# Kernel tuning notes

Measured on AMD Instinct MI355X. Metric: run time of the kernel, lower is better.

## Reference

```python
import jax, jax.numpy as jnp
import numpy as np

N_NODES = 8192
F_DIM = 64
A_DIM = 8
HID = 32
AVG_DEG = 16.0


def _linear_params(key, fan_in, fan_out):
    # torch nn.Linear default init: U(-1/sqrt(fan_in), 1/sqrt(fan_in))
    s = 1.0 / np.sqrt(fan_in)
    k1, k2 = jax.random.split(key)
    W = jax.random.uniform(k1, (fan_in, fan_out), minval=-s, maxval=s, dtype=jnp.float32)
    b = jax.random.uniform(k2, (fan_out,), minval=-s, maxval=s, dtype=jnp.float32)
    return W, b


def setup_inputs() -> dict:
    key = jax.random.key(0)
    ks = jax.random.split(key, 12)
    N, Fd, Ad, H = N_NODES, F_DIM, A_DIM, HID

    features = jax.random.normal(ks[0], (N, Fd), dtype=jnp.float32)
    # sparse symmetric binary adjacency, zero diagonal (edge weights are discarded
    # by the original code -> all edges weight 1, so binary is the faithful form)
    u = jax.random.uniform(ks[1], (N, N), dtype=jnp.float32)
    adj = (u < AVG_DEG / N).astype(jnp.float32)
    adj = jnp.maximum(adj, adj.T) * (1.0 - jnp.eye(N, dtype=jnp.float32))
    mask = jax.random.uniform(ks[2], (N,), dtype=jnp.float32)  # RL_indice (unused)
    action = jax.random.normal(ks[3], (N, Ad), dtype=jnp.float32)

    We1, be1 = _linear_params(ks[4], Fd + Ad, H)
    We2, be2 = _linear_params(ks[5], H, H)
    Wg, bg = _linear_params(ks[6], H, H)      # GCNConv weight + bias
    Wgd, bgd = _linear_params(ks[7], H, H)    # GraphConv_Dense
    Wp1, bp1 = _linear_params(ks[8], 2 * H, H)
    Wp2, bp2 = _linear_params(ks[9], H, H)
    Wv, bv = _linear_params(ks[10], H, 1)

    return dict(features=features, adjacency=adjacency_fix(adj), mask=mask, action=action,
                We1=We1, be1=be1, We2=We2, be2=be2, Wg=Wg, bg=bg, Wgd=Wgd, bgd=bgd,
                Wp1=Wp1, bp1=bp1, Wp2=Wp2, bp2=bp2, Wv=Wv, bv=bv)


def adjacency_fix(adj):
    return adj


def reference(features, adjacency, mask, action,
              We1, be1, We2, be2, Wg, bg, Wgd, bgd,
              Wp1, bp1, Wp2, bp2, Wv, bv):
    # encoder
    X = jax.nn.relu(jnp.concatenate([features, action], axis=1) @ We1 + be1)  # [N,32]
    X = jax.nn.relu(X @ We2 + be2)                                            # [N,32]

    # GCNConv: out = D^{-1/2} (A + I) D^{-1/2} (X W) + b   (self-loops added, deg incl. self)
    deg = jnp.sum(adjacency, axis=1) + 1.0                 # [N]
    dinv = jax.lax.rsqrt(deg)                              # [N]
    S = (X @ Wg) * dinv[:, None]                           # [N,32] scaled messages
    Xg = (adjacency @ S + S) * dinv[:, None] + bg          # aggregate (A@S) + self-loop (S)
    Xg = jax.nn.relu(Xg)
    Xg = jax.nn.relu(Xg @ Wgd + bgd)

    # policy/value head on [graph || encoder] features
    P = jnp.concatenate([Xg, X], axis=1)                   # [N,64]
    P = jax.nn.relu(P @ Wp1 + bp1)
    P = jax.nn.relu(P @ Wp2 + bp2)
    V = P @ Wv + bv                                        # [N,1]
    return V
```

## Files before the change

### kernel.cpp

```cpp
#include <hip/hip_runtime.h>
#include <math.h>

#define NN 8192
#define FD 64
#define AD 8
#define H  32
#define CAP 128

typedef unsigned short u16;

__global__ __launch_bounds__(256) void scan_k(const float4* __restrict__ adj,
                                              u16* __restrict__ nbr,
                                              int* __restrict__ cnt,
                                              float* __restrict__ dinv) {
    const int row = blockIdx.x;
    const float4* arow = adj + (size_t)row * (NN / 4);
    __shared__ int s_cnt;
    if (threadIdx.x == 0) s_cnt = 0;
    __syncthreads();
    u16* myn = nbr + (size_t)row * CAP;

#pragma unroll
    for (int it = 0; it < NN / 4 / 256; ++it) {
        const int i4 = it * 256 + threadIdx.x;
        const float4 v = arow[i4];
        const int nz0 = (v.x != 0.0f), nz1 = (v.y != 0.0f);
        const int nz2 = (v.z != 0.0f), nz3 = (v.w != 0.0f);
        const int local = nz0 + nz1 + nz2 + nz3;
        if (local) {
            int slot = atomicAdd(&s_cnt, local);
            const int base = i4 * 4;
            if (slot + local <= CAP) {
                if (nz0) myn[slot++] = (u16)(base);
                if (nz1) myn[slot++] = (u16)(base + 1);
                if (nz2) myn[slot++] = (u16)(base + 2);
                if (nz3) myn[slot++] = (u16)(base + 3);
            }
        }
    }
    __syncthreads();
    if (threadIdx.x == 0) {
        int c = s_cnt;
        cnt[row]  = (c < CAP) ? c : CAP;
        dinv[row] = 1.0f / sqrtf((float)c + 1.0f);
    }
}

__global__ __launch_bounds__(256) void enc_k(const float* __restrict__ feat,
                                             const float* __restrict__ act,
                                             const float* __restrict__ We1,
                                             const float* __restrict__ be1,
                                             const float* __restrict__ We2,
                                             const float* __restrict__ be2,
                                             const float* __restrict__ Wg,
                                             const float* __restrict__ dinv,
                                             float* __restrict__ X,
                                             float* __restrict__ S) {
    __shared__ float sW1[(FD + AD) * H];
    __shared__ float sb1[H];
    __shared__ float sW2[H * H];
    __shared__ float sb2[H];
    __shared__ float sWg[H * H];
    for (int i = threadIdx.x; i < (FD + AD) * H; i += 256) sW1[i] = We1[i];
    for (int i = threadIdx.x; i < H * H; i += 256) { sW2[i] = We2[i]; sWg[i] = Wg[i]; }
    if (threadIdx.x < H) { sb1[threadIdx.x] = be1[threadIdx.x]; sb2[threadIdx.x] = be2[threadIdx.x]; }
    __syncthreads();

    const int row = blockIdx.x * 256 + threadIdx.x;

    float in[FD + AD];
    const float4* f4 = (const float4*)(feat + (size_t)row * FD);
#pragma unroll
    for (int i = 0; i < FD / 4; ++i) {
        float4 v = f4[i];
        in[4 * i] = v.x; in[4 * i + 1] = v.y; in[4 * i + 2] = v.z; in[4 * i + 3] = v.w;
    }
    const float4* a4 = (const float4*)(act + (size_t)row * AD);
#pragma unroll
    for (int i = 0; i < AD / 4; ++i) {
        float4 v = a4[i];
        in[FD + 4 * i] = v.x; in[FD + 4 * i + 1] = v.y;
        in[FD + 4 * i + 2] = v.z; in[FD + 4 * i + 3] = v.w;
    }

    float h1[H];
#pragma unroll
    for (int o = 0; o < H; ++o) h1[o] = sb1[o];
#pragma unroll
    for (int i = 0; i < FD + AD; ++i) {
        const float xi = in[i];
#pragma unroll
        for (int o = 0; o < H; ++o) h1[o] = fmaf(xi, sW1[i * H + o], h1[o]);
    }
#pragma unroll
    for (int o = 0; o < H; ++o) h1[o] = fmaxf(h1[o], 0.0f);

    float h2[H];
#pragma unroll
    for (int o = 0; o < H; ++o) h2[o] = sb2[o];
#pragma unroll
    for (int i = 0; i < H; ++i) {
        const float xi = h1[i];
#pragma unroll
        for (int o = 0; o < H; ++o) h2[o] = fmaf(xi, sW2[i * H + o], h2[o]);
    }
#pragma unroll
    for (int o = 0; o < H; ++o) h2[o] = fmaxf(h2[o], 0.0f);

    float* Xr = X + (size_t)row * H;
#pragma unroll
    for (int o = 0; o < H; o += 4)
        *(float4*)(Xr + o) = make_float4(h2[o], h2[o + 1], h2[o + 2], h2[o + 3]);

    float t[H];
#pragma unroll
    for (int o = 0; o < H; ++o) t[o] = 0.0f;
#pragma unroll
    for (int i = 0; i < H; ++i) {
        const float xi = h2[i];
#pragma unroll
        for (int o = 0; o < H; ++o) t[o] = fmaf(xi, sWg[i * H + o], t[o]);
    }
    const float di = dinv[row];
    float* Sr = S + (size_t)row * H;
#pragma unroll
    for (int o = 0; o < H; o += 4)
        *(float4*)(Sr + o) = make_float4(t[o] * di, t[o + 1] * di, t[o + 2] * di, t[o + 3] * di);
}

__global__ __launch_bounds__(256) void fin_k(const float* __restrict__ S,
                                             const float* __restrict__ X,
                                             const u16* __restrict__ nbr,
                                             const int* __restrict__ cnt,
                                             const float* __restrict__ dinv,
                                             const float* __restrict__ bg,
                                             const float* __restrict__ Wgd,
                                             const float* __restrict__ bgd,
                                             const float* __restrict__ Wp1,
                                             const float* __restrict__ bp1,
                                             const float* __restrict__ Wp2,
                                             const float* __restrict__ bp2,
                                             const float* __restrict__ Wv,
                                             const float* __restrict__ bv,
                                             float* __restrict__ out) {
    __shared__ float sbg[H];
    __shared__ float sWgd[H * H];
    __shared__ float sbgd[H];
    __shared__ float sWp1[2 * H * H];
    __shared__ float sbp1[H];
    __shared__ float sWp2[H * H];
    __shared__ float sbp2[H];
    __shared__ float sWv[H];
    __shared__ float sbv;
    for (int i = threadIdx.x; i < H * H; i += 256) { sWgd[i] = Wgd[i]; sWp2[i] = Wp2[i]; }
    for (int i = threadIdx.x; i < 2 * H * H; i += 256) sWp1[i] = Wp1[i];
    if (threadIdx.x < H) {
        sbg[threadIdx.x]  = bg[threadIdx.x];
        sbgd[threadIdx.x] = bgd[threadIdx.x];
        sbp1[threadIdx.x] = bp1[threadIdx.x];
        sbp2[threadIdx.x] = bp2[threadIdx.x];
        sWv[threadIdx.x]  = Wv[threadIdx.x];
    }
    if (threadIdx.x == 0) sbv = bv[0];
    __syncthreads();

    const int row = blockIdx.x * 256 + threadIdx.x;

    float acc[H];
    const float4* Sr = (const float4*)(S + (size_t)row * H);
#pragma unroll
    for (int q = 0; q < H / 4; ++q) {
        float4 v = Sr[q];
        acc[4 * q] = v.x; acc[4 * q + 1] = v.y; acc[4 * q + 2] = v.z; acc[4 * q + 3] = v.w;
    }
    const int n = cnt[row];
    const u16* myn = nbr + (size_t)row * CAP;
    for (int e = 0; e < n; ++e) {
        const int j = myn[e];
        const float4* Sj = (const float4*)(S + (size_t)j * H);
#pragma unroll
        for (int q = 0; q < H / 4; ++q) {
            float4 v = Sj[q];
            acc[4 * q] += v.x; acc[4 * q + 1] += v.y;
            acc[4 * q + 2] += v.z; acc[4 * q + 3] += v.w;
        }
    }

    const float di = dinv[row];
    float xg[H];
#pragma unroll
    for (int k = 0; k < H; ++k) xg[k] = fmaxf(fmaf(acc[k], di, sbg[k]), 0.0f);

    float xg2[H];
#pragma unroll
    for (int o = 0; o < H; ++o) xg2[o] = sbgd[o];
#pragma unroll
    for (int k = 0; k < H; ++k) {
        const float xk = xg[k];
#pragma unroll
        for (int o = 0; o < H; ++o) xg2[o] = fmaf(xk, sWgd[k * H + o], xg2[o]);
    }
#pragma unroll
    for (int o = 0; o < H; ++o) xg2[o] = fmaxf(xg2[o], 0.0f);

    float x[H];
    const float4* Xr = (const float4*)(X + (size_t)row * H);
#pragma unroll
    for (int q = 0; q < H / 4; ++q) {
        float4 v = Xr[q];
        x[4 * q] = v.x; x[4 * q + 1] = v.y; x[4 * q + 2] = v.z; x[4 * q + 3] = v.w;
    }

    float p1[H];
#pragma unroll
    for (int o = 0; o < H; ++o) p1[o] = sbp1[o];
#pragma unroll
    for (int k = 0; k < H; ++k) {
        const float xk = xg2[k];
#pragma unroll
        for (int o = 0; o < H; ++o) p1[o] = fmaf(xk, sWp1[k * H + o], p1[o]);
    }
#pragma unroll
    for (int k = 0; k < H; ++k) {
        const float xk = x[k];
#pragma unroll
        for (int o = 0; o < H; ++o) p1[o] = fmaf(xk, sWp1[(H + k) * H + o], p1[o]);
    }
#pragma unroll
    for (int o = 0; o < H; ++o) p1[o] = fmaxf(p1[o], 0.0f);

    float p2[H];
#pragma unroll
    for (int o = 0; o < H; ++o) p2[o] = sbp2[o];
#pragma unroll
    for (int k = 0; k < H; ++k) {
        const float xk = p1[k];
#pragma unroll
        for (int o = 0; o < H; ++o) p2[o] = fmaf(xk, sWp2[k * H + o], p2[o]);
    }

    float v = sbv;
#pragma unroll
    for (int k = 0; k < H; ++k) v = fmaf(fmaxf(p2[k], 0.0f), sWv[k], v);

    out[row] = v;
}

extern "C" void kernel_launch(void* const* d_in, const int* in_sizes, int n_in,
                              void* d_out, int out_size, void* d_ws, size_t ws_size,
                              hipStream_t stream) {
    (void)in_sizes; (void)n_in; (void)out_size; (void)ws_size;

    const float* feat = (const float*)d_in[0];
    const float* adj  = (const float*)d_in[1];
    const float* act  = (const float*)d_in[3];
    const float* We1  = (const float*)d_in[4];
    const float* be1  = (const float*)d_in[5];
    const float* We2  = (const float*)d_in[6];
    const float* be2  = (const float*)d_in[7];
    const float* Wg   = (const float*)d_in[8];
    const float* bg   = (const float*)d_in[9];
    const float* Wgd  = (const float*)d_in[10];
    const float* bgd  = (const float*)d_in[11];
    const float* Wp1  = (const float*)d_in[12];
    const float* bp1  = (const float*)d_in[13];
    const float* Wp2  = (const float*)d_in[14];
    const float* bp2  = (const float*)d_in[15];
    const float* Wv   = (const float*)d_in[16];
    const float* bv   = (const float*)d_in[17];

    char* ws = (char*)d_ws;
    u16*   nbr  = (u16*)ws;
    char*  p    = ws + (size_t)NN * CAP * sizeof(u16);
    int*   cnt  = (int*)p;            p += (size_t)NN * 4;
    float* dinv = (float*)p;          p += (size_t)NN * 4;
    float* X    = (float*)p;          p += (size_t)NN * H * 4;
    float* S    = (float*)p;

    float* out = (float*)d_out;

    scan_k<<<NN, 256, 0, stream>>>((const float4*)adj, nbr, cnt, dinv);
    enc_k<<<NN / 256, 256, 0, stream>>>(feat, act, We1, be1, We2, be2, Wg, dinv, X, S);
    fin_k<<<NN / 256, 256, 0, stream>>>(S, X, nbr, cnt, dinv, bg, Wgd, bgd,
                                        Wp1, bp1, Wp2, bp2, Wv, bv, out);
}
```

Baseline: 528.2 us.

## Merge adjacency scan and encoder into one launch, apply dinv during aggregation

Folds the adjacency scan and the encoder MLP into a single kernel: the first NN blocks scan adjacency rows and the extra blocks run the encoder. This works because the encoder no longer needs dinv, since the scaling by dinv[j] moves into the neighbor gather in fin_k. The scan also preloads all eight float4 loads per thread before processing them, to raise memory-level parallelism. fin_k drops to 64-thread blocks so more blocks spread across CUs, at the cost of an extra dinv load per edge.

```diff
diff --git a/kernel.cpp b/kernel.cpp
--- a/kernel.cpp
+++ b/kernel.cpp
@@ -9,140 +9,151 @@
 
 typedef unsigned short u16;
 
-__global__ __launch_bounds__(256) void scan_k(const float4* __restrict__ adj,
-                                              u16* __restrict__ nbr,
-                                              int* __restrict__ cnt,
-                                              float* __restrict__ dinv) {
-    const int row = blockIdx.x;
-    const float4* arow = adj + (size_t)row * (NN / 4);
-    __shared__ int s_cnt;
-    if (threadIdx.x == 0) s_cnt = 0;
-    __syncthreads();
-    u16* myn = nbr + (size_t)row * CAP;
-
-#pragma unroll
-    for (int it = 0; it < NN / 4 / 256; ++it) {
-        const int i4 = it * 256 + threadIdx.x;
-        const float4 v = arow[i4];
-        const int nz0 = (v.x != 0.0f), nz1 = (v.y != 0.0f);
-        const int nz2 = (v.z != 0.0f), nz3 = (v.w != 0.0f);
-        const int local = nz0 + nz1 + nz2 + nz3;
-        if (local) {
-            int slot = atomicAdd(&s_cnt, local);
-            const int base = i4 * 4;
-            if (slot + local <= CAP) {
-                if (nz0) myn[slot++] = (u16)(base);
-                if (nz1) myn[slot++] = (u16)(base + 1);
-                if (nz2) myn[slot++] = (u16)(base + 2);
-                if (nz3) myn[slot++] = (u16)(base + 3);
-            }
-        }
-    }
-    __syncthreads();
-    if (threadIdx.x == 0) {
-        int c = s_cnt;
-        cnt[row]  = (c < CAP) ? c : CAP;
-        dinv[row] = 1.0f / sqrtf((float)c + 1.0f);
-    }
-}
-
-__global__ __launch_bounds__(256) void enc_k(const float* __restrict__ feat,
+#define OW1 0
+#define OW2 2304
+#define OWG 3328
+#define OB1 4352
+#define OB2 4384
+#define SMEM_FLOATS 4416
+
+__global__ __launch_bounds__(256) void pre_k(const float4* __restrict__ adj,
+                                             const float* __restrict__ feat,
                                              const float* __restrict__ act,
                                              const float* __restrict__ We1,
                                              const float* __restrict__ be1,
                                              const float* __restrict__ We2,
                                              const float* __restrict__ be2,
                                              const float* __restrict__ Wg,
-                                             const float* __restrict__ dinv,
+                                             u16* __restrict__ nbr,
+                                             int* __restrict__ cnt,
+                                             float* __restrict__ dinv,
                                              float* __restrict__ X,
-                                             float* __restrict__ S) {
-    __shared__ float sW1[(FD + AD) * H];
-    __shared__ float sb1[H];
-    __shared__ float sW2[H * H];
-    __shared__ float sb2[H];
-    __shared__ float sWg[H * H];
-    for (int i = threadIdx.x; i < (FD + AD) * H; i += 256) sW1[i] = We1[i];
-    for (int i = threadIdx.x; i < H * H; i += 256) { sW2[i] = We2[i]; sWg[i] = Wg[i]; }
-    if (threadIdx.x < H) { sb1[threadIdx.x] = be1[threadIdx.x]; sb2[threadIdx.x] = be2[threadIdx.x]; }
-    __syncthreads();
-
-    const int row = blockIdx.x * 256 + threadIdx.x;
-
-    float in[FD + AD];
-    const float4* f4 = (const float4*)(feat + (size_t)row * FD);
-#pragma unroll
-    for (int i = 0; i < FD / 4; ++i) {
-        float4 v = f4[i];
-        in[4 * i] = v.x; in[4 * i + 1] = v.y; in[4 * i + 2] = v.z; in[4 * i + 3] = v.w;
-    }
-    const float4* a4 = (const float4*)(act + (size_t)row * AD);
-#pragma unroll
-    for (int i = 0; i < AD / 4; ++i) {
-        float4 v = a4[i];
-        in[FD + 4 * i] = v.x; in[FD + 4 * i + 1] = v.y;
-        in[FD + 4 * i + 2] = v.z; in[FD + 4 * i + 3] = v.w;
-    }
-
-    float h1[H];
-#pragma unroll
-    for (int o = 0; o < H; ++o) h1[o] = sb1[o];
-#pragma unroll
-    for (int i = 0; i < FD + AD; ++i) {
-        const float xi = in[i];
-#pragma unroll
-        for (int o = 0; o < H; ++o) h1[o] = fmaf(xi, sW1[i * H + o], h1[o]);
-    }
-#pragma unroll
-    for (int o = 0; o < H; ++o) h1[o] = fmaxf(h1[o], 0.0f);
-
-    float h2[H];
-#pragma unroll
-    for (int o = 0; o < H; ++o) h2[o] = sb2[o];
-#pragma unroll
-    for (int i = 0; i < H; ++i) {
-        const float xi = h1[i];
-#pragma unroll
-        for (int o = 0; o < H; ++o) h2[o] = fmaf(xi, sW2[i * H + o], h2[o]);
-    }
-#pragma unroll
-    for (int o = 0; o < H; ++o) h2[o] = fmaxf(h2[o], 0.0f);
-
-    float* Xr = X + (size_t)row * H;
-#pragma unroll
-    for (int o = 0; o < H; o += 4)
-        *(float4*)(Xr + o) = make_float4(h2[o], h2[o + 1], h2[o + 2], h2[o + 3]);
-
-    float t[H];
-#pragma unroll
-    for (int o = 0; o < H; ++o) t[o] = 0.0f;
-#pragma unroll
-    for (int i = 0; i < H; ++i) {
-        const float xi = h2[i];
-#pragma unroll
-        for (int o = 0; o < H; ++o) t[o] = fmaf(xi, sWg[i * H + o], t[o]);
-    }
-    const float di = dinv[row];
-    float* Sr = S + (size_t)row * H;
-#pragma unroll
-    for (int o = 0; o < H; o += 4)
-        *(float4*)(Sr + o) = make_float4(t[o] * di, t[o + 1] * di, t[o + 2] * di, t[o + 3] * di);
+                                             float* __restrict__ T) {
+    __shared__ float smem[SMEM_FLOATS];
+
+    if (blockIdx.x < NN) {
+        int* s_cnt = (int*)smem;
+        const int row = blockIdx.x;
+        const float4* arow = adj + (size_t)row * (NN / 4);
+        if (threadIdx.x == 0) *s_cnt = 0;
+        __syncthreads();
+
+        float4 v[8];
+#pragma unroll
+        for (int it = 0; it < 8; ++it) v[it] = arow[it * 256 + threadIdx.x];
+
+        u16* myn = nbr + (size_t)row * CAP;
+#pragma unroll
+        for (int it = 0; it < 8; ++it) {
+            const int base = (it * 256 + threadIdx.x) * 4;
+            const int nz0 = (v[it].x != 0.0f), nz1 = (v[it].y != 0.0f);
+            const int nz2 = (v[it].z != 0.0f), nz3 = (v[it].w != 0.0f);
+            const int local = nz0 + nz1 + nz2 + nz3;
+            if (local) {
+                int slot = atomicAdd(s_cnt, local);
+                if (slot + local <= CAP) {
+                    if (nz0) myn[slot++] = (u16)(base);
+                    if (nz1) myn[slot++] = (u16)(base + 1);
+                    if (nz2) myn[slot++] = (u16)(base + 2);
+                    if (nz3) myn[slot++] = (u16)(base + 3);
+                }
+            }
+        }
+        __syncthreads();
+        if (threadIdx.x == 0) {
+            const int c = *s_cnt;
+            cnt[row]  = (c < CAP) ? c : CAP;
+            dinv[row] = 1.0f / sqrtf((float)c + 1.0f);
+        }
+    } else {
+        for (int i = threadIdx.x; i < (FD + AD) * H; i += 256) smem[OW1 + i] = We1[i];
+        for (int i = threadIdx.x; i < H * H; i += 256) {
+            smem[OW2 + i] = We2[i];
+            smem[OWG + i] = Wg[i];
+        }
+        if (threadIdx.x < H) {
+            smem[OB1 + threadIdx.x] = be1[threadIdx.x];
+            smem[OB2 + threadIdx.x] = be2[threadIdx.x];
+        }
+        __syncthreads();
+
+        const int row = (blockIdx.x - NN) * 256 + threadIdx.x;
+
+        float in[FD + AD];
+        const float4* f4 = (const float4*)(feat + (size_t)row * FD);
+#pragma unroll
+        for (int i = 0; i < FD / 4; ++i) {
+            float4 v = f4[i];
+            in[4 * i] = v.x; in[4 * i + 1] = v.y; in[4 * i + 2] = v.z; in[4 * i + 3] = v.w;
+        }
+        const float4* a4 = (const float4*)(act + (size_t)row * AD);
+#pragma unroll
+        for (int i = 0; i < AD / 4; ++i) {
+            float4 v = a4[i];
+            in[FD + 4 * i] = v.x; in[FD + 4 * i + 1] = v.y;
+            in[FD + 4 * i + 2] = v.z; in[FD + 4 * i + 3] = v.w;
+        }
+
+        float h1[H];
+#pragma unroll
+        for (int o = 0; o < H; ++o) h1[o] = smem[OB1 + o];
+#pragma unroll
+        for (int i = 0; i < FD + AD; ++i) {
+            const float xi = in[i];
+#pragma unroll
+            for (int o = 0; o < H; ++o) h1[o] = fmaf(xi, smem[OW1 + i * H + o], h1[o]);
+        }
+#pragma unroll
+        for (int o = 0; o < H; ++o) h1[o] = fmaxf(h1[o], 0.0f);
+
+        float h2[H];
+#pragma unroll
+        for (int o = 0; o < H; ++o) h2[o] = smem[OB2 + o];
+#pragma unroll
+        for (int i = 0; i < H; ++i) {
+            const float xi = h1[i];
+#pragma unroll
+            for (int o = 0; o < H; ++o) h2[o] = fmaf(xi, smem[OW2 + i * H + o], h2[o]);
+        }
+#pragma unroll
+        for (int o = 0; o < H; ++o) h2[o] = fmaxf(h2[o], 0.0f);
+
+        float* Xr = X + (size_t)row * H;
+#pragma unroll
+        for (int o = 0; o < H; o += 4)
+            *(float4*)(Xr + o) = make_float4(h2[o], h2[o + 1], h2[o + 2], h2[o + 3]);
+
+        float t[H];
+#pragma unroll
+        for (int o = 0; o < H; ++o) t[o] = 0.0f;
+#pragma unroll
+        for (int i = 0; i < H; ++i) {
+            const float xi = h2[i];
+#pragma unroll
+            for (int o = 0; o < H; ++o) t[o] = fmaf(xi, smem[OWG + i * H + o], t[o]);
+        }
+        float* Tr = T + (size_t)row * H;
+#pragma unroll
+        for (int o = 0; o < H; o += 4)
+            *(float4*)(Tr + o) = make_float4(t[o], t[o + 1], t[o + 2], t[o + 3]);
+    }
 }
 
-__global__ __launch_bounds__(256) void fin_k(const float* __restrict__ S,
-                                             const float* __restrict__ X,
-                                             const u16* __restrict__ nbr,
-                                             const int* __restrict__ cnt,
-                                             const float* __restrict__ dinv,
-                                             const float* __restrict__ bg,
-                                             const float* __restrict__ Wgd,
-                                             const float* __restrict__ bgd,
-                                             const float* __restrict__ Wp1,
-                                             const float* __restrict__ bp1,
-                                             const float* __restrict__ Wp2,
-                                             const float* __restrict__ bp2,
-                                             const float* __restrict__ Wv,
-                                             const float* __restrict__ bv,
-                                             float* __restrict__ out) {
+__global__ __launch_bounds__(64) void fin_k(const float* __restrict__ T,
+                                            const float* __restrict__ X,
+                                            const u16* __restrict__ nbr,
+                                            const int* __restrict__ cnt,
+                                            const float* __restrict__ dinv,
+                                            const float* __restrict__ bg,
+                                            const float* __restrict__ Wgd,
+                                            const float* __restrict__ bgd,
+                                            const float* __restrict__ Wp1,
+                                            const float* __restrict__ bp1,
+                                            const float* __restrict__ Wp2,
+                                            const float* __restrict__ bp2,
+                                            const float* __restrict__ Wv,
+                                            const float* __restrict__ bv,
+                                            float* __restrict__ out) {
     __shared__ float sbg[H];
     __shared__ float sWgd[H * H];
     __shared__ float sbgd[H];
@@ -152,8 +163,8 @@
     __shared__ float sbp2[H];
     __shared__ float sWv[H];
     __shared__ float sbv;
-    for (int i = threadIdx.x; i < H * H; i += 256) { sWgd[i] = Wgd[i]; sWp2[i] = Wp2[i]; }
-    for (int i = threadIdx.x; i < 2 * H * H; i += 256) sWp1[i] = Wp1[i];
+    for (int i = threadIdx.x; i < H * H; i += 64) { sWgd[i] = Wgd[i]; sWp2[i] = Wp2[i]; }
+    for (int i = threadIdx.x; i < 2 * H * H; i += 64) sWp1[i] = Wp1[i];
     if (threadIdx.x < H) {
         sbg[threadIdx.x]  = bg[threadIdx.x];
         sbgd[threadIdx.x] = bgd[threadIdx.x];
@@ -164,29 +175,33 @@
     if (threadIdx.x == 0) sbv = bv[0];
     __syncthreads();
 
-    const int row = blockIdx.x * 256 + threadIdx.x;
+    const int row = blockIdx.x * 64 + threadIdx.x;
+    const float di = dinv[row];
 
     float acc[H];
-    const float4* Sr = (const float4*)(S + (size_t)row * H);
+    const float4* Tr = (const float4*)(T + (size_t)row * H);
 #pragma unroll
     for (int q = 0; q < H / 4; ++q) {
-        float4 v = Sr[q];
-        acc[4 * q] = v.x; acc[4 * q + 1] = v.y; acc[4 * q + 2] = v.z; acc[4 * q + 3] = v.w;
+        float4 v = Tr[q];
+        acc[4 * q]     = v.x * di; acc[4 * q + 1] = v.y * di;
+        acc[4 * q + 2] = v.z * di; acc[4 * q + 3] = v.w * di;
     }
     const int n = cnt[row];
     const u16* myn = nbr + (size_t)row * CAP;
     for (int e = 0; e < n; ++e) {
         const int j = myn[e];
-        const float4* Sj = (const float4*)(S + (size_t)j * H);
+        const float dj = dinv[j];
+        const float4* Tj = (const float4*)(T + (size_t)j * H);
 #pragma unroll
         for (int q = 0; q < H / 4; ++q) {
-            float4 v = Sj[q];
-            acc[4 * q] += v.x; acc[4 * q + 1] += v.y;
-            acc[4 * q + 2] += v.z; acc[4 * q + 3] += v.w;
-        }
-    }
-
-    const float di = dinv[row];
+            float4 v = Tj[q];
+            acc[4 * q]     = fmaf(v.x, dj, acc[4 * q]);
+            acc[4 * q + 1] = fmaf(v.y, dj, acc[4 * q + 1]);
+            acc[4 * q + 2] = fmaf(v.z, dj, acc[4 * q + 2]);
+            acc[4 * q + 3] = fmaf(v.w, dj, acc[4 * q + 3]);
+        }
+    }
+
     float xg[H];
 #pragma unroll
     for (int k = 0; k < H; ++k) xg[k] = fmaxf(fmaf(acc[k], di, sbg[k]), 0.0f);
@@ -275,12 +290,13 @@
     int*   cnt  = (int*)p;            p += (size_t)NN * 4;
     float* dinv = (float*)p;          p += (size_t)NN * 4;
     float* X    = (float*)p;          p += (size_t)NN * H * 4;
-    float* S    = (float*)p;
+    float* T    = (float*)p;
 
     float* out = (float*)d_out;
 
-    scan_k<<<NN, 256, 0, stream>>>((const float4*)adj, nbr, cnt, dinv);
-    enc_k<<<NN / 256, 256, 0, stream>>>(feat, act, We1, be1, We2, be2, Wg, dinv, X, S);
-    fin_k<<<NN / 256, 256, 0, stream>>>(S, X, nbr, cnt, dinv, bg, Wgd, bgd,
-                                        Wp1, bp1, Wp2, bp2, Wv, bv, out);
+    pre_k<<<NN + NN / 256, 256, 0, stream>>>((const float4*)adj, feat, act,
+                                             We1, be1, We2, be2, Wg,
+                                             nbr, cnt, dinv, X, T);
+    fin_k<<<NN / 64, 64, 0, stream>>>(T, X, nbr, cnt, dinv, bg, Wgd, bgd,
+                                      Wp1, bp1, Wp2, bp2, Wv, bv, out);
 }
```

Result: faster. 455.4 us (-13.8%).
